# Optimization experiments

Measured on AMD Instinct MI355X. Metric: run time of the kernel, lower is better.

## Reference

```python
import jax, jax.numpy as jnp
import numpy as np

S, B, T, H, K, FH, OUT = 4, 256, 256, 128, 5, 48, 1
DW, AW = 64, 32            # dynamics-MLP width, attention width
EPS_BN, EPS_U = 1e-5, 1e-6


def setup_inputs() -> dict:
    key = jax.random.key(0)
    ks = jax.random.split(key, 16)
    r = lambda i, shape, s: jax.random.normal(ks[i], shape, jnp.float32) * s
    return {
        "x": jax.random.normal(ks[0], (B, 1, T), jnp.float32),
        "t_span": jnp.linspace(0.0, 1.0, T, dtype=jnp.float32),
        # decomposer: per-scale DynamicDilationConv + BN + ReLU + Conv1d + BN + ReLU
        "c1w": r(1, (S, 1, 1, K), 0.3), "c1b": jnp.zeros((S, 1)),
        "bn1_g": jnp.ones((S, 1)), "bn1_b": jnp.zeros((S, 1)),
        "c2w": r(2, (S, 1, 1, K), 0.3), "c2b": jnp.zeros((S, 1)),
        "bn2_g": jnp.ones((S, 1)), "bn2_b": jnp.zeros((S, 1)),
        # per-scale ProbabilisticNeuralDynamics MLP: (H+1+1) -> 64 -> 2H
        "dw1": r(3, (S, H + 2, DW), 0.1), "db1": jnp.zeros((S, DW)),
        "dw2": r(4, (S, DW, 2 * H), 0.1), "db2": jnp.zeros((S, 2 * H)),
        # fusion attention H -> 32 -> 1
        "a1w": r(5, (H, AW), 0.1), "a1b": jnp.zeros((AW,)),
        "a2w": r(6, (AW, 1), 0.1), "a2b": jnp.zeros((1,)),
        # GRU (torch layout: W_ih [3H, in], W_hh [3H, H])
        "wih": r(7, (3 * H, OUT), 0.1), "whh": r(8, (3 * H, H), 0.05),
        "bih": jnp.zeros((3 * H,)), "bhh": jnp.zeros((3 * H,)),
        "fcw": r(9, (H, OUT), 0.1), "fcb": jnp.zeros((OUT,)),
        "lvw": r(10, (H, OUT), 0.1), "lvb": jnp.zeros((OUT,)),
        "init_token": jnp.zeros((1, OUT)),
    }


def _conv1d(x, w, b):
    # x:[B,C,L], w:[O,I,K]; dilation = round(clamp(exp(log_dilation=0),1)) = 1
    pad = (w.shape[-1] - 1) // 2
    y = jax.lax.conv_general_dilated(x, w, (1,), [(pad, pad)],
                                     dimension_numbers=("NCH", "OIH", "NCH"))
    return y + b[None, :, None]


def _bn(x, g, b):
    # BatchNorm1d in training mode: batch stats over (N, L)
    m = x.mean(axis=(0, 2), keepdims=True)
    v = x.var(axis=(0, 2), keepdims=True)
    return g[None, :, None] * (x - m) * jax.lax.rsqrt(v + EPS_BN) + b[None, :, None]


def _decompose(x, c1w, c1b, g1, b1, c2w, c2b, g2, b2):
    h = jnp.maximum(_bn(_conv1d(x, c1w, c1b), g1, b1), 0.0)
    h = jnp.maximum(_bn(_conv1d(h, c2w, c2b), g2, b2), 0.0)
    return h  # [B,1,T]


def _ode_scale(xseq, t_span, w1, b1, w2, b2):
    # xseq:[B,T,1]; integrate (mu, logvar) with RK4 on the t_span grid
    def f(t, h):
        idx = jnp.argmin(jnp.abs(t_span - t))
        x_t = jnp.take(xseq, idx, axis=1)                 # [B,1]
        tf = t * jnp.ones((h.shape[0], 1), h.dtype)       # time feature
        u = jnp.maximum(jnp.concatenate([h, x_t, tf], -1) @ w1 + b1, 0.0) @ w2 + b2
        return u[:, :H], u[:, H:]

    def step(carry, ts):
        h, lv = carry
        t0, t1 = ts
        dt = t1 - t0
        k1m, k1v = f(t0, h)
        k2m, k2v = f(t0 + dt / 2, h + dt / 2 * k1m)
        k3m, k3v = f(t0 + dt / 2, h + dt / 2 * k2m)
        k4m, k4v = f(t1, h + dt * k3m)
        h = h + dt / 6 * (k1m + 2 * k2m + 2 * k3m + k4m)
        lv = lv + dt / 6 * (k1v + 2 * k2v + 2 * k3v + k4v)
        return (h, lv), None

    z = jnp.zeros((xseq.shape[0], H), xseq.dtype)
    (h, lv), _ = jax.lax.scan(step, (z, z), (t_span[:-1], t_span[1:]))
    return h, lv  # final-time latent, matching h_sol[:, -1, :]


def _forward(x, t_span, c1w, c1b, bn1_g, bn1_b, c2w, c2b, bn2_g, bn2_b,
             dw1, db1, dw2, db2, a1w, a1b, a2w, a2b,
             wih, whh, bih, bhh, fcw, fcb, lvw, lvb, init_token):
    # multi-scale decomposition -> [S,B,1,T]
    comps = jax.vmap(_decompose, in_axes=(None, 0, 0, 0, 0, 0, 0, 0, 0))(
        x, c1w, c1b, bn1_g, bn1_b, c2w, c2b, bn2_g, bn2_b)
    xseqs = comps[:, :, 0, :, None]                       # [S,B,T,1]
    means, logvars = jax.vmap(_ode_scale, in_axes=(0, None, 0, 0, 0, 0))(
        xseqs, t_span, dw1, db1, dw2, db2)                # each [S,B,H]
    means = jnp.transpose(means, (1, 0, 2))               # [B,S,H]
    logvars = jnp.transpose(logvars, (1, 0, 2))
    # uncertainty-scaled attention fusion
    scores = jnp.maximum(means @ a1w + a1b, 0.0) @ a2w + a2b        # [B,S,1]
    uncert = jnp.mean(jnp.exp(logvars), axis=-1, keepdims=True)     # [B,S,1]
    weights = jax.nn.softmax(scores / (uncert + EPS_U), axis=1)
    fused = jnp.sum(weights * means, axis=1)              # [B,H]

    def dec_step(carry, _):
        h, tok = carry
        gi = tok @ wih.T + bih
        gh = h @ whh.T + bhh
        ir, iz, inn = jnp.split(gi, 3, axis=-1)
        hr, hz, hn = jnp.split(gh, 3, axis=-1)
        r = jax.nn.sigmoid(ir + hr)
        zz = jax.nn.sigmoid(iz + hz)
        n = jnp.tanh(inn + r * hn)
        h = (1.0 - zz) * n + zz * h
        pred = h @ fcw + fcb
        plv = h @ lvw + lvb
        return (h, pred), (pred, plv)

    tok0 = jnp.broadcast_to(init_token, (fused.shape[0], OUT))
    _, (outs, lvs) = jax.lax.scan(dec_step, (fused, tok0), None, length=FH)
    return jnp.transpose(outs, (1, 0, 2)), jnp.transpose(lvs, (1, 0, 2))


def reference(x, t_span, c1w, c1b, bn1_g, bn1_b, c2w, c2b, bn2_g, bn2_b,
              dw1, db1, dw2, db2, a1w, a1b, a2w, a2b,
              wih, whh, bih, bhh, fcw, fcb, lvw, lvb, init_token):
    return _forward(x, t_span, c1w, c1b, bn1_g, bn1_b, c2w, c2b, bn2_g, bn2_b,
                    dw1, db1, dw2, db2, a1w, a1b, a2w, a2b,
                    wih, whh, bih, bhh, fcw, fcb, lvw, lvb, init_token)
```

## Files before the change

### kernel.cpp

```cpp
#include <hip/hip_runtime.h>
#include <math.h>

#define NS   4
#define NB   256
#define NT   256
#define NH   128
#define NDW  64
#define NFH  48

__global__ __launch_bounds__(256) void k_d1(
    const float* __restrict__ x,
    const float* __restrict__ c1w, const float* __restrict__ c1b,
    float* __restrict__ tmpA, double* __restrict__ pp1)
{
    const int s     = blockIdx.x >> 6;
    const int chunk = blockIdx.x & 63;
    const int tid   = threadIdx.x;
    __shared__ double wred[4][2];

    float w[5];
#pragma unroll
    for (int k = 0; k < 5; ++k) w[k] = c1w[s*5 + k];
    const float cb = c1b[s];

    double ls = 0.0, lq = 0.0;
#pragma unroll
    for (int r = 0; r < 4; ++r) {
        const int bb = chunk*4 + r;
        const float* xb = x + bb*NT;
        float acc = cb;
#pragma unroll
        for (int k = 0; k < 5; ++k) {
            int tt = tid + k - 2;
            if (tt >= 0 && tt < NT) acc += xb[tt] * w[k];
        }
        tmpA[s*65536 + bb*NT + tid] = acc;
        ls += (double)acc; lq += (double)acc * (double)acc;
    }
#pragma unroll
    for (int off = 32; off > 0; off >>= 1) {
        ls += __shfl_xor(ls, off); lq += __shfl_xor(lq, off);
    }
    if ((tid & 63) == 0) { wred[tid>>6][0] = ls; wred[tid>>6][1] = lq; }
    __syncthreads();
    if (tid == 0) {
        pp1[(s*64 + chunk)*2 + 0] = wred[0][0]+wred[1][0]+wred[2][0]+wred[3][0];
        pp1[(s*64 + chunk)*2 + 1] = wred[0][1]+wred[1][1]+wred[2][1]+wred[3][1];
    }
}

__global__ __launch_bounds__(256) void k_d3(
    const float* __restrict__ tmpA, const double* __restrict__ pp1,
    const float* __restrict__ g1,  const float* __restrict__ b1,
    const float* __restrict__ c2w, const float* __restrict__ c2b,
    float* __restrict__ cv2, double* __restrict__ pp2)
{
    const int s     = blockIdx.x >> 6;
    const int chunk = blockIdx.x & 63;
    const int tid   = threadIdx.x;
    __shared__ float hsh[256];
    __shared__ double wred[4][2];

    double lsum = 0.0, lsq = 0.0;
    for (int q = 0; q < 64; ++q) {
        lsum += pp1[(s*64 + q)*2 + 0];
        lsq  += pp1[(s*64 + q)*2 + 1];
    }
    const double Nn = 65536.0;
    double mm = lsum / Nn;
    double vv = lsq / Nn - mm*mm;
    const float m1 = (float)mm, rs1 = (float)(1.0 / sqrt(vv + 1e-5));
    const float A1 = g1[s]*rs1, B1 = b1[s] - g1[s]*m1*rs1;

    float w[5];
#pragma unroll
    for (int k = 0; k < 5; ++k) w[k] = c2w[s*5 + k];
    const float cb = c2b[s];

    double ls = 0.0, lq = 0.0;
    for (int r = 0; r < 4; ++r) {
        const int bb = chunk*4 + r;
        float y = tmpA[s*65536 + bb*NT + tid];
        hsh[tid] = fmaxf(fmaf(A1, y, B1), 0.f);
        __syncthreads();
        float acc = cb;
#pragma unroll
        for (int k = 0; k < 5; ++k) {
            int tt = tid + k - 2;
            if (tt >= 0 && tt < NT) acc += hsh[tt] * w[k];
        }
        cv2[s*65536 + bb*NT + tid] = acc;
        ls += (double)acc; lq += (double)acc * (double)acc;
        __syncthreads();
    }
#pragma unroll
    for (int off = 32; off > 0; off >>= 1) {
        ls += __shfl_xor(ls, off); lq += __shfl_xor(lq, off);
    }
    if ((tid & 63) == 0) { wred[tid>>6][0] = ls; wred[tid>>6][1] = lq; }
    __syncthreads();
    if (tid == 0) {
        pp2[(s*64 + chunk)*2 + 0] = wred[0][0]+wred[1][0]+wred[2][0]+wred[3][0];
        pp2[(s*64 + chunk)*2 + 1] = wred[0][1]+wred[1][1]+wred[2][1]+wred[3][1];
    }
}

__global__ __launch_bounds__(64) void k_mat(
    const float* __restrict__ dw1, const float* __restrict__ dw2,
    const float* __restrict__ db2, const float* __restrict__ tspan,
    float* __restrict__ Mt, float* __restrict__ bM,
    int* __restrict__ imid_g, float* __restrict__ Tg)
{
    if (blockIdx.x == 256) {
        __shared__ float ts[256];
        const int t = threadIdx.x;
        for (int e = t; e < 256; e += 64) ts[e] = tspan[e];
        __syncthreads();
        for (int i = t; i < 255; i += 64) {
            float t0 = ts[i], t1 = ts[i+1];
            float tm = t0 + (t1 - t0) * 0.5f;
            int best = 0; float bd = fabsf(ts[0] - tm);
            for (int j = 1; j < 256; ++j) {
                float d = fabsf(ts[j] - tm);
                if (d < bd) { bd = d; best = j; }
            }
            imid_g[i] = best;
        }
        if (t == 0) {
            float T = 0.f;
            for (int i = 0; i < 255; ++i) T += (ts[i+1] - ts[i]);
            Tg[0] = T;
        }
        return;
    }
    const int s = blockIdx.x >> 6;
    const int c = blockIdx.x & 63;
    const int k = threadIdx.x;
    __shared__ float col[128];

    col[k]      = dw1[(s*130 + k)*64 + c];
    col[k + 64] = dw1[(s*130 + 64 + k)*64 + c];
    __syncthreads();

    const float4* dp = (const float4*)(dw2 + (s*64 + k)*256);
    double acc = 0.0;
#pragma unroll 8
    for (int j4 = 0; j4 < 32; ++j4) {
        float4 dv = dp[j4];
        acc += (double)dv.x * (double)col[4*j4+0]
             + (double)dv.y * (double)col[4*j4+1]
             + (double)dv.z * (double)col[4*j4+2]
             + (double)dv.w * (double)col[4*j4+3];
    }
    Mt[(s*64 + c)*64 + k] = (float)acc;

    double pb = (double)db2[s*256 + k]      * (double)col[k]
              + (double)db2[s*256 + 64 + k] * (double)col[k + 64];
#pragma unroll
    for (int off = 32; off > 0; off >>= 1) pb += __shfl_xor(pb, off);
    if (k == 0) bM[s*64 + c] = (float)pb;
}

__device__ __forceinline__ float rlf(float v, int l) {
    return __int_as_float(__builtin_amdgcn_readlane(__float_as_int(v), l));
}
__device__ __forceinline__ float pick4f(float r0, float r1, float r2, float r3, int i) {
    int l = i & 63, h = i >> 6;
    float a = (h & 2) ? ((h & 1) ? r3 : r2) : ((h & 1) ? r1 : r0);
    return rlf(a, l);
}
__device__ __forceinline__ int pick4i(int r0, int r1, int r2, int r3, int i) {
    int l = i & 63, h = i >> 6;
    int a = (h & 2) ? ((h & 1) ? r3 : r2) : ((h & 1) ? r1 : r0);
    return __builtin_amdgcn_readlane(a, l);
}
__device__ __forceinline__ float dot64_lds(const float* __restrict__ u1s,
                                           const float* __restrict__ Mc,
                                           float bMc) {
    float d0 = bMc, d1 = 0.f, d2 = 0.f, d3 = 0.f;
    const float4* up = (const float4*)u1s;
#pragma unroll
    for (int g = 0; g < 16; ++g) {
        float4 uv = up[g];
        d0 = fmaf(uv.x, Mc[4*g+0], d0);
        d1 = fmaf(uv.y, Mc[4*g+1], d1);
        d2 = fmaf(uv.z, Mc[4*g+2], d2);
        d3 = fmaf(uv.w, Mc[4*g+3], d3);
    }
    return (d0 + d1) + (d2 + d3);
}

__global__ __attribute__((amdgpu_waves_per_eu(1, 1)))
__launch_bounds__(64) void k_ode(
    const float* __restrict__ cv2, const double* __restrict__ pp2,
    const float* __restrict__ g2,  const float* __restrict__ b2,
    const float* __restrict__ tspan, const int* __restrict__ imid_g,
    const float* __restrict__ Mt, const float* __restrict__ bM_g,
    const float* __restrict__ dw1, const float* __restrict__ db1,
    float* __restrict__ S_g)
{
    const int b   = blockIdx.x;
    const int s   = b >> 8;
    const int row = b & 255;
    const int c   = threadIdx.x;

    __shared__ __align__(16) float u1s[64];

    double lsum = 0.0, lsq = 0.0;
    for (int q = 0; q < 64; ++q) {
        lsum += pp2[(s*64 + q)*2 + 0];
        lsq  += pp2[(s*64 + q)*2 + 1];
    }
    const double Nn = 65536.0;
    double mm = lsum / Nn;
    double vv = lsq / Nn - mm*mm;
    const float m2 = (float)mm, rs2 = (float)(1.0 / sqrt(vv + 1e-5));
    const float A2 = g2[s]*rs2, B2 = b2[s] - g2[s]*m2*rs2;

    const float* __restrict__ xrow = cv2 + (s*NB + row)*NT;

    float ts0 = tspan[c],       ts1 = tspan[64 + c];
    float ts2 = tspan[128 + c], ts3 = tspan[192 + c];
    float xr0 = fmaxf(fmaf(A2, xrow[c],       B2), 0.f);
    float xr1 = fmaxf(fmaf(A2, xrow[64 + c],  B2), 0.f);
    float xr2 = fmaxf(fmaf(A2, xrow[128 + c], B2), 0.f);
    float xr3 = fmaxf(fmaf(A2, xrow[192 + c], B2), 0.f);
    int   im0 = imid_g[c];
    int   im1 = imid_g[64 + c];
    int   im2 = imid_g[128 + c];
    int   im3 = (192 + c < 255) ? imid_g[192 + c] : 0;

    const float bMc = bM_g[s*64 + c];
    const float b1c = db1[s*64 + c];
    const float w1x = dw1[(s*130 + 128)*64 + c];
    const float w1t = dw1[(s*130 + 129)*64 + c];

    float Mc[64];
    const float4* mp = (const float4*)(Mt + (s*64 + c)*64);
#pragma unroll
    for (int j = 0; j < 16; ++j) {
        float4 t = mp[j];
        Mc[4*j+0] = t.x; Mc[4*j+1] = t.y; Mc[4*j+2] = t.z; Mc[4*j+3] = t.w;
    }
#pragma unroll
    for (int j = 0; j < 64; ++j) asm volatile("" : "+v"(Mc[j]));

    float a = 0.f;
    float S = 0.f;

    for (int i = 0; i < 255; ++i) {
        float t0 = pick4f(ts0, ts1, ts2, ts3, i);
        float t1 = pick4f(ts0, ts1, ts2, ts3, i + 1);
        float dt = t1 - t0;
        int   im = pick4i(im0, im1, im2, im3, i);
        float xi = pick4f(xr0, xr1, xr2, xr3, i);
        float xm = pick4f(xr0, xr1, xr2, xr3, im);
        float x1 = pick4f(xr0, xr1, xr2, xr3, i + 1);
        float tm = t0 + dt * 0.5f;
        float hdt = dt * 0.5f;

        float u11 = fmaxf(a + b1c + xi*w1x + t0*w1t, 0.f);
        u1s[c] = u11;
        float v1  = dot64_lds(u1s, Mc, bMc);

        float u12 = fmaxf(fmaf(hdt, v1, a) + b1c + xm*w1x + tm*w1t, 0.f);
        u1s[c] = u12;
        float v2  = dot64_lds(u1s, Mc, bMc);

        float u13 = fmaxf(fmaf(hdt, v2, a) + b1c + xm*w1x + tm*w1t, 0.f);
        u1s[c] = u13;
        float v3  = dot64_lds(u1s, Mc, bMc);

        float u14 = fmaxf(fmaf(dt, v3, a) + b1c + x1*w1x + t1*w1t, 0.f);
        u1s[c] = u14;
        float v4  = dot64_lds(u1s, Mc, bMc);

        float d6 = dt * (1.0f / 6.0f);
        a += d6 * ((v1 + v4) + 2.f*(v2 + v3));
        S += d6 * ((u11 + u14) + 2.f*(u12 + u13));
    }

    S_g[(s*256 + row)*64 + c] = S;
}

__global__ __launch_bounds__(384, 1) void k_gru(
    const float* __restrict__ S_g, const float* __restrict__ dw2,
    const float* __restrict__ db2, const float* __restrict__ Tg,
    const float* __restrict__ a1w, const float* __restrict__ a1b,
    const float* __restrict__ a2w, const float* __restrict__ a2b,
    const float* __restrict__ wih, const float* __restrict__ whh,
    const float* __restrict__ bih, const float* __restrict__ bhh,
    const float* __restrict__ fcw, const float* __restrict__ fcb,
    const float* __restrict__ lvw, const float* __restrict__ lvb,
    const float* __restrict__ init_token, float* __restrict__ out)
{
    const int b   = blockIdx.x;
    const int tid = threadIdx.x;

    __shared__ __align__(16) float Ssh[4][64];
    __shared__ __align__(16) float msh[4][128];
    __shared__ __align__(16) float evs[4][128];
    __shared__ __align__(16) float hl[128];
    __shared__ float ghl[384];
    __shared__ float scoreL[4];
    __shared__ float unc_part[2][4];
    __shared__ float wgt[4];
    __shared__ float redL[2][2];
    __shared__ float tokL;

    if (tid < 256) {
        int s = tid >> 6, cc = tid & 63;
        Ssh[s][cc] = S_g[(s*256 + b)*64 + cc];
    }
    const float T = Tg[0];
    __syncthreads();

    for (int e = tid; e < 1024; e += 384) {
        int s = e >> 8, j = e & 255;
        float acc = T * db2[s*256 + j];
        const float4* s4 = (const float4*)Ssh[s];
#pragma unroll
        for (int k4 = 0; k4 < 16; ++k4) {
            float4 sv = s4[k4];
            acc += sv.x * dw2[(s*64 + 4*k4 + 0)*256 + j]
                 + sv.y * dw2[(s*64 + 4*k4 + 1)*256 + j]
                 + sv.z * dw2[(s*64 + 4*k4 + 2)*256 + j]
                 + sv.w * dw2[(s*64 + 4*k4 + 3)*256 + j];
        }
        if (j < 128) msh[s][j] = acc;
        else         evs[s][j - 128] = expf(acc);
    }
    __syncthreads();

    if (tid < 128) {
        int wv = tid >> 6;
#pragma unroll
        for (int s = 0; s < 4; ++s) {
            float v = evs[s][tid];
#pragma unroll
            for (int off = 32; off > 0; off >>= 1) v += __shfl_xor(v, off);
            if ((tid & 63) == 0) unc_part[wv][s] = v;
        }
    }
    if (tid < 128) {
        int s = tid >> 5, aq = tid & 31;
        float hd = a1b[aq];
#pragma unroll 4
        for (int i = 0; i < 128; ++i) hd += msh[s][i] * a1w[i*32 + aq];
        hd = fmaxf(hd, 0.f);
        float sc = hd * a2w[aq];
#pragma unroll
        for (int off = 16; off > 0; off >>= 1) sc += __shfl_xor(sc, off);
        if (aq == 0) scoreL[s] = sc + a2b[0];
    }
    __syncthreads();
    if (tid == 0) {
        float sv[4], mx = -1e30f;
#pragma unroll
        for (int s = 0; s < 4; ++s) {
            float u = (unc_part[0][s] + unc_part[1][s]) / 128.f;
            sv[s] = scoreL[s] / (u + 1e-6f);
            mx = fmaxf(mx, sv[s]);
        }
        float se = 0.f, ev[4];
#pragma unroll
        for (int s = 0; s < 4; ++s) { ev[s] = expf(sv[s] - mx); se += ev[s]; }
#pragma unroll
        for (int s = 0; s < 4; ++s) wgt[s] = ev[s] / se;
        tokL = init_token[0];
    }
    __syncthreads();
    if (tid < 128) {
        float f = 0.f;
#pragma unroll
        for (int s = 0; s < 4; ++s) f += wgt[s] * msh[s][tid];
        hl[tid] = f;
    }

    float4 whh4[32];
    const float4* wr = (const float4*)(whh + tid*128);
#pragma unroll
    for (int k = 0; k < 32; ++k) whh4[k] = wr[k];
    float bhhj = bhh[tid];
    float wih_r = 0.f, wih_z = 0.f, wih_n = 0.f;
    float bih_r = 0.f, bih_z = 0.f, bih_n = 0.f;
    float fcwi = 0.f, lvwi = 0.f;
    if (tid < 128) {
        wih_r = wih[tid]; wih_z = wih[128+tid]; wih_n = wih[256+tid];
        bih_r = bih[tid]; bih_z = bih[128+tid]; bih_n = bih[256+tid];
        fcwi  = fcw[tid]; lvwi  = lvw[tid];
    }
    const float fcbv = fcb[0], lvbv = lvb[0];
    __syncthreads();

    for (int t = 0; t < NFH; ++t) {
        float g0 = 0.f, g1 = 0.f, g2 = 0.f, g3 = 0.f;
        const float4* h4 = (const float4*)hl;
#pragma unroll
        for (int k = 0; k < 32; ++k) {
            float4 hv = h4[k];
            float4 wvv = whh4[k];
            g0 += hv.x * wvv.x; g1 += hv.y * wvv.y;
            g2 += hv.z * wvv.z; g3 += hv.w * wvv.w;
        }
        ghl[tid] = ((g0 + g1) + (g2 + g3)) + bhhj;
        __syncthreads();

        if (tid < 128) {
            float tok = tokL;
            float r  = 1.f / (1.f + expf(-(tok*wih_r + bih_r + ghl[tid])));
            float zz = 1.f / (1.f + expf(-(tok*wih_z + bih_z + ghl[128+tid])));
            float n  = tanhf(tok*wih_n + bih_n + r * ghl[256+tid]);
            float hn = (1.f - zz) * n + zz * hl[tid];
            hl[tid] = hn;
            float pp = hn * fcwi, pl = hn * lvwi;
#pragma unroll
            for (int off = 32; off > 0; off >>= 1) {
                pp += __shfl_xor(pp, off);
                pl += __shfl_xor(pl, off);
            }
            int wvx = tid >> 6;
            if ((tid & 63) == 0) { redL[wvx][0] = pp; redL[wvx][1] = pl; }
        }
        __syncthreads();
        if (tid == 0) {
            float pr = redL[0][0] + redL[1][0] + fcbv;
            float pv = redL[0][1] + redL[1][1] + lvbv;
            out[b*NFH + t] = pr;
            out[NB*NFH + b*NFH + t] = pv;
            tokL = pr;
        }
        __syncthreads();
    }
}

extern "C" void kernel_launch(void* const* d_in, const int* in_sizes, int n_in,
                              void* d_out, int out_size, void* d_ws, size_t ws_size,
                              hipStream_t stream)
{
    const float* x      = (const float*)d_in[0];
    const float* tspan  = (const float*)d_in[1];
    const float* c1w    = (const float*)d_in[2];
    const float* c1b    = (const float*)d_in[3];
    const float* bn1g   = (const float*)d_in[4];
    const float* bn1b   = (const float*)d_in[5];
    const float* c2w    = (const float*)d_in[6];
    const float* c2b    = (const float*)d_in[7];
    const float* bn2g   = (const float*)d_in[8];
    const float* bn2b   = (const float*)d_in[9];
    const float* dw1    = (const float*)d_in[10];
    const float* db1    = (const float*)d_in[11];
    const float* dw2    = (const float*)d_in[12];
    const float* db2    = (const float*)d_in[13];
    const float* a1w    = (const float*)d_in[14];
    const float* a1b    = (const float*)d_in[15];
    const float* a2w    = (const float*)d_in[16];
    const float* a2b    = (const float*)d_in[17];
    const float* wih    = (const float*)d_in[18];
    const float* whh    = (const float*)d_in[19];
    const float* bih    = (const float*)d_in[20];
    const float* bhh    = (const float*)d_in[21];
    const float* fcw    = (const float*)d_in[22];
    const float* fcb    = (const float*)d_in[23];
    const float* lvw    = (const float*)d_in[24];
    const float* lvb    = (const float*)d_in[25];
    const float* itok   = (const float*)d_in[26];

    float* ws    = (float*)d_ws;
    float*  cv2  = ws;
    float*  tmpA = ws + 262144;
    float*  S_g  = ws + 524288;
    float*  Mt   = ws + 589824;
    float*  bMg  = ws + 606208;
    float*  Tg   = ws + 606464;
    int*    imid = (int*)(ws + 606720);
    double* pp1  = (double*)(ws + 606976);
    double* pp2  = (double*)(ws + 608000);

    k_d1<<<256, 256, 0, stream>>>(x, c1w, c1b, tmpA, pp1);
    k_mat<<<257, 64, 0, stream>>>(dw1, dw2, db2, tspan, Mt, bMg, imid, Tg);
    k_d3<<<256, 256, 0, stream>>>(tmpA, pp1, bn1g, bn1b, c2w, c2b, cv2, pp2);
    k_ode<<<1024, 64, 0, stream>>>(cv2, pp2, bn2g, bn2b, tspan, imid,
                                   Mt, bMg, dw1, db1, S_g);
    k_gru<<<256, 384, 0, stream>>>(S_g, dw2, db2, Tg, a1w, a1b, a2w, a2b,
                                   wih, whh, bih, bhh, fcw, fcb, lvw, lvb,
                                   itok, (float*)d_out);
}
```

Before: 421.5 us.

## Replace LDS dot-product broadcast with bpermute and DPP row rotations in ODE kernel

The per-stage 64-wide matrix-vector product in the RK4 loop no longer writes each lane's activation to LDS and reads it back as float4 broadcasts. Instead it gathers four 16-lane groups with ds_bpermute and cycles values inside each row using DPP row_ror, with Mt rows stored in a permuted order that matches the rotation. The per-step input samples (x, midpoint x) are now precomputed into LDS, and t values are read directly, replacing the readlane pick chains. The goal is to shorten the serial latency of each RK4 stage, at the cost of relying on exact DPP rotation semantics matching the permuted weight layout.

```diff
diff --git a/kernel.cpp b/kernel.cpp
--- a/kernel.cpp
+++ b/kernel.cpp
@@ -152,7 +152,8 @@
              + (double)dv.z * (double)col[4*j4+2]
              + (double)dv.w * (double)col[4*j4+3];
     }
-    Mt[(s*64 + c)*64 + k] = (float)acc;
+    const int slot = (k & 48) | (((c & 15) - (k & 15)) & 15);
+    Mt[(s*64 + c)*64 + slot] = (float)acc;
 
     double pb = (double)db2[s*256 + k]      * (double)col[k]
               + (double)db2[s*256 + 64 + k] * (double)col[k + 64];
@@ -161,32 +162,29 @@
     if (k == 0) bM[s*64 + c] = (float)pb;
 }
 
-__device__ __forceinline__ float rlf(float v, int l) {
-    return __int_as_float(__builtin_amdgcn_readlane(__float_as_int(v), l));
-}
-__device__ __forceinline__ float pick4f(float r0, float r1, float r2, float r3, int i) {
-    int l = i & 63, h = i >> 6;
-    float a = (h & 2) ? ((h & 1) ? r3 : r2) : ((h & 1) ? r1 : r0);
-    return rlf(a, l);
-}
-__device__ __forceinline__ int pick4i(int r0, int r1, int r2, int r3, int i) {
-    int l = i & 63, h = i >> 6;
-    int a = (h & 2) ? ((h & 1) ? r3 : r2) : ((h & 1) ? r1 : r0);
-    return __builtin_amdgcn_readlane(a, l);
-}
-__device__ __forceinline__ float dot64_lds(const float* __restrict__ u1s,
-                                           const float* __restrict__ Mc,
-                                           float bMc) {
-    float d0 = bMc, d1 = 0.f, d2 = 0.f, d3 = 0.f;
-    const float4* up = (const float4*)u1s;
-#pragma unroll
-    for (int g = 0; g < 16; ++g) {
-        float4 uv = up[g];
-        d0 = fmaf(uv.x, Mc[4*g+0], d0);
-        d1 = fmaf(uv.y, Mc[4*g+1], d1);
-        d2 = fmaf(uv.z, Mc[4*g+2], d2);
-        d3 = fmaf(uv.w, Mc[4*g+3], d3);
-    }
+__device__ __forceinline__ float bperm(int addr, float v) {
+    return __int_as_float(__builtin_amdgcn_ds_bpermute(addr, __float_as_int(v)));
+}
+#define ROR(x, p) __int_as_float(__builtin_amdgcn_update_dpp( \
+    0, __float_as_int(x), 0x120 + (p), 0xF, 0xF, false))
+
+__device__ __forceinline__ float dotDPP(float u, const float* __restrict__ Mc,
+                                        float bMc, int A0, int A1, int A2, int A3)
+{
+    float u0 = bperm(A0, u), u1 = bperm(A1, u);
+    float u2 = bperm(A2, u), u3 = bperm(A3, u);
+    float d0 = fmaf(u0, Mc[0], bMc);
+    float d1 = u1 * Mc[16];
+    float d2 = u2 * Mc[32];
+    float d3 = u3 * Mc[48];
+#define STEP(p) \
+    d0 = fmaf(ROR(u0, p), Mc[p],      d0); \
+    d1 = fmaf(ROR(u1, p), Mc[16+(p)], d1); \
+    d2 = fmaf(ROR(u2, p), Mc[32+(p)], d2); \
+    d3 = fmaf(ROR(u3, p), Mc[48+(p)], d3);
+    STEP(1)  STEP(2)  STEP(3)  STEP(4)  STEP(5)  STEP(6)  STEP(7)  STEP(8)
+    STEP(9)  STEP(10) STEP(11) STEP(12) STEP(13) STEP(14) STEP(15)
+#undef STEP
     return (d0 + d1) + (d2 + d3);
 }
 
@@ -202,9 +200,10 @@
     const int b   = blockIdx.x;
     const int s   = b >> 8;
     const int row = b & 255;
-    const int c   = threadIdx.x;
-
-    __shared__ __align__(16) float u1s[64];
+    const int l   = threadIdx.x;
+
+    __shared__ __align__(16) float xls[256];
+    __shared__ __align__(16) float xms[256];
 
     double lsum = 0.0, lsq = 0.0;
     for (int q = 0; q < 64; ++q) {
@@ -215,28 +214,27 @@
     double mm = lsum / Nn;
     double vv = lsq / Nn - mm*mm;
     const float m2 = (float)mm, rs2 = (float)(1.0 / sqrt(vv + 1e-5));
-    const float A2 = g2[s]*rs2, B2 = b2[s] - g2[s]*m2*rs2;
+    const float bnA = g2[s]*rs2, bnB = b2[s] - g2[s]*m2*rs2;
 
     const float* __restrict__ xrow = cv2 + (s*NB + row)*NT;
-
-    float ts0 = tspan[c],       ts1 = tspan[64 + c];
-    float ts2 = tspan[128 + c], ts3 = tspan[192 + c];
-    float xr0 = fmaxf(fmaf(A2, xrow[c],       B2), 0.f);
-    float xr1 = fmaxf(fmaf(A2, xrow[64 + c],  B2), 0.f);
-    float xr2 = fmaxf(fmaf(A2, xrow[128 + c], B2), 0.f);
-    float xr3 = fmaxf(fmaf(A2, xrow[192 + c], B2), 0.f);
-    int   im0 = imid_g[c];
-    int   im1 = imid_g[64 + c];
-    int   im2 = imid_g[128 + c];
-    int   im3 = (192 + c < 255) ? imid_g[192 + c] : 0;
-
-    const float bMc = bM_g[s*64 + c];
-    const float b1c = db1[s*64 + c];
-    const float w1x = dw1[(s*130 + 128)*64 + c];
-    const float w1t = dw1[(s*130 + 129)*64 + c];
+#pragma unroll
+    for (int q = 0; q < 4; ++q)
+        xls[64*q + l] = fmaxf(fmaf(bnA, xrow[64*q + l], bnB), 0.f);
+    __syncthreads();
+#pragma unroll
+    for (int q = 0; q < 4; ++q) {
+        int idx = 64*q + l;
+        if (idx < 255) xms[idx] = xls[imid_g[idx]];
+    }
+    __syncthreads();
+
+    const float bMc = bM_g[s*64 + l];
+    const float b1c = db1[s*64 + l];
+    const float w1x = dw1[(s*130 + 128)*64 + l];
+    const float w1t = dw1[(s*130 + 129)*64 + l];
 
     float Mc[64];
-    const float4* mp = (const float4*)(Mt + (s*64 + c)*64);
+    const float4* mp = (const float4*)(Mt + (s*64 + l)*64);
 #pragma unroll
     for (int j = 0; j < 16; ++j) {
         float4 t = mp[j];
@@ -245,42 +243,37 @@
 #pragma unroll
     for (int j = 0; j < 64; ++j) asm volatile("" : "+v"(Mc[j]));
 
+    const int lm = (l & 15) << 2;
+    const int A0 = lm, A1 = lm + 64, A2 = lm + 128, A3 = lm + 192;
+
     float a = 0.f;
     float S = 0.f;
 
     for (int i = 0; i < 255; ++i) {
-        float t0 = pick4f(ts0, ts1, ts2, ts3, i);
-        float t1 = pick4f(ts0, ts1, ts2, ts3, i + 1);
-        float dt = t1 - t0;
-        int   im = pick4i(im0, im1, im2, im3, i);
-        float xi = pick4f(xr0, xr1, xr2, xr3, i);
-        float xm = pick4f(xr0, xr1, xr2, xr3, im);
-        float x1 = pick4f(xr0, xr1, xr2, xr3, i + 1);
-        float tm = t0 + dt * 0.5f;
-        float hdt = dt * 0.5f;
+        const float t0 = tspan[i];
+        const float t1 = tspan[i+1];
+        const float dt = t1 - t0;
+        const float tm = t0 + dt * 0.5f;
+        const float hdt = dt * 0.5f;
+        const float xi  = xls[i];
+        const float x1v = xls[i+1];
+        const float xm  = xms[i];
 
         float u11 = fmaxf(a + b1c + xi*w1x + t0*w1t, 0.f);
-        u1s[c] = u11;
-        float v1  = dot64_lds(u1s, Mc, bMc);
-
+        float v1  = dotDPP(u11, Mc, bMc, A0, A1, A2, A3);
         float u12 = fmaxf(fmaf(hdt, v1, a) + b1c + xm*w1x + tm*w1t, 0.f);
-        u1s[c] = u12;
-        float v2  = dot64_lds(u1s, Mc, bMc);
-
+        float v2  = dotDPP(u12, Mc, bMc, A0, A1, A2, A3);
         float u13 = fmaxf(fmaf(hdt, v2, a) + b1c + xm*w1x + tm*w1t, 0.f);
-        u1s[c] = u13;
-        float v3  = dot64_lds(u1s, Mc, bMc);
-
-        float u14 = fmaxf(fmaf(dt, v3, a) + b1c + x1*w1x + t1*w1t, 0.f);
-        u1s[c] = u14;
-        float v4  = dot64_lds(u1s, Mc, bMc);
+        float v3  = dotDPP(u13, Mc, bMc, A0, A1, A2, A3);
+        float u14 = fmaxf(fmaf(dt, v3, a) + b1c + x1v*w1x + t1*w1t, 0.f);
+        float v4  = dotDPP(u14, Mc, bMc, A0, A1, A2, A3);
 
         float d6 = dt * (1.0f / 6.0f);
         a += d6 * ((v1 + v4) + 2.f*(v2 + v3));
         S += d6 * ((u11 + u14) + 2.f*(u12 + u13));
     }
 
-    S_g[(s*256 + row)*64 + c] = S;
+    S_g[(s*256 + row)*64 + l] = S;
 }
 
 __global__ __launch_bounds__(384, 1) void k_gru(
```

Result: slower. 471.6 us (+11.9%).
